# Kernel optimization log

Hardware: AMD Instinct MI355X
Metric: run time of the kernel (lower is better)

## Reference

```python
import jax, jax.numpy as jnp
import numpy as np
from jax import lax

I, H, C = 1086, 16, 15


def _lstm_layer(x, w_ih, w_hh, b):
    # x: [B, T, in], w_ih: [4H, in], w_hh: [4H, H], b: [4H]  (b = b_ih + b_hh)
    B = x.shape[0]
    Hd = w_hh.shape[1]
    # precompute the big input projection outside the scan
    pre = jnp.einsum('bti,gi->btg', x, w_ih) + b  # [B, T, 4H]

    def step(carry, pt):
        h, c = carry
        gates = pt + h @ w_hh.T  # [B, 4H]
        i, f, g, o = jnp.split(gates, 4, axis=-1)  # torch gate order i,f,g,o
        i = jax.nn.sigmoid(i)
        f = jax.nn.sigmoid(f)
        g = jnp.tanh(g)
        o = jax.nn.sigmoid(o)
        c = f * c + i * g
        h = o * jnp.tanh(c)
        return (h, c), h

    h0 = jnp.zeros((B, Hd), x.dtype)
    c0 = jnp.zeros((B, Hd), x.dtype)
    _, ys = lax.scan(step, (h0, c0), jnp.swapaxes(pre, 0, 1))
    return jnp.swapaxes(ys, 0, 1)  # [B, T, H]


def setup_inputs() -> dict:
    key = jax.random.key(0)
    ks = jax.random.split(key, 20)
    s = 1.0 / np.sqrt(H)  # torch LSTM/Linear default init scale
    x = jax.random.normal(ks[0], (256, 200, I), dtype=jnp.float32)

    def w(k, shape):
        return jax.random.uniform(k, shape, jnp.float32, -s, s)

    inp = {'x': x}
    ins = [I, H, H, H]  # lstm1 layer0/1, lstm2 layer0/1
    names = ['l0a', 'l0b', 'l1a', 'l1b']
    ki = 1
    for n, d_in in zip(names, ins):
        inp['w_ih_' + n] = w(ks[ki], (4 * H, d_in)); ki += 1
        inp['w_hh_' + n] = w(ks[ki], (4 * H, H)); ki += 1
        inp['b_' + n] = w(ks[ki], (4 * H,)); ki += 1
    inp['w_fc1'] = w(ks[ki], (H, H)); ki += 1
    inp['b_fc1'] = w(ks[ki], (H,)); ki += 1
    inp['w_fc2'] = w(ks[ki], (C, H)); ki += 1
    inp['b_fc2'] = w(ks[ki], (C,))
    return inp


def reference(x, w_ih_l0a, w_hh_l0a, b_l0a, w_ih_l0b, w_hh_l0b, b_l0b,
              w_ih_l1a, w_hh_l1a, b_l1a, w_ih_l1b, w_hh_l1b, b_l1b,
              w_fc1, b_fc1, w_fc2, b_fc2):
    # lstm1 (2 layers), dropout between layers is identity in eval mode
    out = _lstm_layer(x, w_ih_l0a, w_hh_l0a, b_l0a)
    out = _lstm_layer(out, w_ih_l0b, w_hh_l0b, b_l0b)
    # lstm2 (2 layers)
    out = _lstm_layer(out, w_ih_l1a, w_hh_l1a, b_l1a)
    out = _lstm_layer(out, w_ih_l1b, w_hh_l1b, b_l1b)
    h_last = out[:, -1, :]  # [B, H]
    h = jax.nn.relu(h_last @ w_fc1.T + b_fc1)
    logits = h @ w_fc2.T + b_fc2  # [B, C]
    return jax.nn.softmax(logits, axis=1)
```

## Files before the change

kernel.cpp:

```cpp
#include <hip/hip_runtime.h>

#define T_STEPS 200
#define IN_DIM 1086
#define KTILES 34
#define M_TOTAL 51200

using f32x4v = __attribute__((ext_vector_type(4))) float;
using bf16x8 = __attribute__((ext_vector_type(8))) short;
using u32x4  = __attribute__((ext_vector_type(4))) unsigned int;
typedef unsigned uv2 __attribute__((ext_vector_type(2)));

#if __has_builtin(__builtin_amdgcn_permlane16_swap) && __has_builtin(__builtin_amdgcn_permlane32_swap)
#define HAVE_PERMLANE_SWAP 1
#else
#define HAVE_PERMLANE_SWAP 0
#endif

#if __has_builtin(__builtin_amdgcn_exp2f)
#define EXP2F(x) __builtin_amdgcn_exp2f(x)
#else
#define EXP2F(x) exp2f(x)
#endif

__device__ __forceinline__ float rl_f(float v, int lane) {
    return __uint_as_float((unsigned)__builtin_amdgcn_readlane((int)__float_as_uint(v), lane));
}

__global__ __launch_bounds__(256) void prepack_w(
    const float* __restrict__ W,
    unsigned short* __restrict__ Wh, unsigned short* __restrict__ Wl)
{
    int idx = blockIdx.x * 256 + threadIdx.x;
    if (idx >= KTILES * 4 * 64 * 8) return;
    int j = idx & 7;
    int n = (idx >> 3) & 63;
    int k = (idx >> 9) * 8 + j;
    float v = (k < IN_DIM) ? W[n * IN_DIM + k] : 0.0f;
    unsigned u = __float_as_uint(v);
    unsigned hi = u & 0xffff0000u;
    float lo = v - __uint_as_float(hi);
    Wh[idx] = (unsigned short)(u >> 16);
    Wl[idx] = (unsigned short)(__float_as_uint(lo) >> 16);
}

__device__ __forceinline__ void cvt_hilo(const float a[8], bf16x8& hv, bf16x8& lv) {
    union { u32x4 u; bf16x8 v; } H, L;
    #pragma unroll
    for (int p = 0; p < 4; ++p) {
        float a0 = a[2 * p], a1 = a[2 * p + 1];
        unsigned u0 = __float_as_uint(a0), u1 = __float_as_uint(a1);
        unsigned h0 = u0 & 0xffff0000u, h1 = u1 & 0xffff0000u;
        H.u[p] = (u0 >> 16) | h1;
        float l0 = a0 - __uint_as_float(h0);
        float l1 = a1 - __uint_as_float(h1);
        L.u[p] = (__float_as_uint(l0) >> 16) | (__float_as_uint(l1) & 0xffff0000u);
    }
    hv = H.v; lv = L.v;
}

__global__ __launch_bounds__(64) void pre0_gemm(
    const float* __restrict__ X,
    const unsigned short* __restrict__ Wh, const unsigned short* __restrict__ Wl,
    const float* __restrict__ bias, float* __restrict__ out)
{
    const int lane = threadIdx.x;
    const int fr = lane & 15;
    const int kg = lane >> 4;
    const long m0 = (long)blockIdx.x * 32;

    const float* xr0 = X + (m0 + fr) * (long)IN_DIM;
    const float* xr1 = X + (m0 + 16 + fr) * (long)IN_DIM;

    f32x4v acc[2][4];
    #pragma unroll
    for (int mf = 0; mf < 2; ++mf)
        #pragma unroll
        for (int nf = 0; nf < 4; ++nf)
            #pragma unroll
            for (int r = 0; r < 4; ++r) acc[mf][nf][r] = 0.0f;

    for (int kt = 0; kt < KTILES; ++kt) {
        const int kb = kt * 32 + kg * 8;

        float a0[8], a1[8];
        if (kt < KTILES - 1) {
            #pragma unroll
            for (int q = 0; q < 4; ++q) {
                float2 t0 = *(const float2*)(xr0 + kb + 2 * q);
                float2 t1 = *(const float2*)(xr1 + kb + 2 * q);
                a0[2 * q] = t0.x; a0[2 * q + 1] = t0.y;
                a1[2 * q] = t1.x; a1[2 * q + 1] = t1.y;
            }
        } else {
            #pragma unroll
            for (int j = 0; j < 8; ++j) {
                int k = kb + j;
                a0[j] = (k < IN_DIM) ? xr0[k] : 0.0f;
                a1[j] = (k < IN_DIM) ? xr1[k] : 0.0f;
            }
        }

        const long bbase = (long)(kt * 4 + kg) * 64 * 8;
        bf16x8 bh[4], bl[4];
        #pragma unroll
        for (int nf = 0; nf < 4; ++nf) {
            bh[nf] = *(const bf16x8*)(Wh + bbase + (nf * 16 + fr) * 8);
            bl[nf] = *(const bf16x8*)(Wl + bbase + (nf * 16 + fr) * 8);
        }

        bf16x8 ah0, al0, ah1, al1;
        cvt_hilo(a0, ah0, al0);
        cvt_hilo(a1, ah1, al1);

        #pragma unroll
        for (int nf = 0; nf < 4; ++nf) {
            acc[0][nf] = __builtin_amdgcn_mfma_f32_16x16x32_bf16(ah0, bh[nf], acc[0][nf], 0, 0, 0);
            acc[0][nf] = __builtin_amdgcn_mfma_f32_16x16x32_bf16(al0, bh[nf], acc[0][nf], 0, 0, 0);
            acc[0][nf] = __builtin_amdgcn_mfma_f32_16x16x32_bf16(ah0, bl[nf], acc[0][nf], 0, 0, 0);
            acc[1][nf] = __builtin_amdgcn_mfma_f32_16x16x32_bf16(ah1, bh[nf], acc[1][nf], 0, 0, 0);
            acc[1][nf] = __builtin_amdgcn_mfma_f32_16x16x32_bf16(al1, bh[nf], acc[1][nf], 0, 0, 0);
            acc[1][nf] = __builtin_amdgcn_mfma_f32_16x16x32_bf16(ah1, bl[nf], acc[1][nf], 0, 0, 0);
        }
    }

    float bvv[4];
    #pragma unroll
    for (int nf = 0; nf < 4; ++nf) bvv[nf] = bias[nf * 16 + fr];
    #pragma unroll
    for (int mf = 0; mf < 2; ++mf)
        #pragma unroll
        for (int nf = 0; nf < 4; ++nf)
            #pragma unroll
            for (int r = 0; r < 4; ++r) {
                long row = m0 + mf * 16 + kg * 4 + r;
                out[row * 64 + nf * 16 + fr] = acc[mf][nf][r] + bvv[nf];
            }
}

__global__ __launch_bounds__(256) void mega_scan(
    const float* __restrict__ pre0, const float* __restrict__ whh0,
    const float* __restrict__ wih1, const float* __restrict__ whh1, const float* __restrict__ b1,
    const float* __restrict__ wih2, const float* __restrict__ whh2, const float* __restrict__ b2,
    const float* __restrict__ wih3, const float* __restrict__ whh3, const float* __restrict__ b3,
    const float* __restrict__ w_fc1, const float* __restrict__ b_fc1,
    const float* __restrict__ w_fc2, const float* __restrict__ b_fc2,
    float* __restrict__ out)
{
    __shared__ float buf[3][T_STEPS][16];

    const int b    = blockIdx.x;
    const int tid  = threadIdx.x;
    const int g    = tid & 63;
    const int wv   = tid >> 6;

    bool sel16 = false, sel32 = false;
#if HAVE_PERMLANE_SWAP
    {
        uv2 q16 = __builtin_amdgcn_permlane16_swap((unsigned)g, (unsigned)g, false, false);
        sel16 = (__builtin_amdgcn_readfirstlane((int)q16[1]) == 16);
        uv2 q32 = __builtin_amdgcn_permlane32_swap((unsigned)g, (unsigned)g, false, false);
        sel32 = (__builtin_amdgcn_readfirstlane((int)q32[1]) == 32);
    }
#endif

    const float* wih = nullptr; const float* whh; const float* bias = nullptr;
    if      (wv == 0) { whh = whh0; }
    else if (wv == 1) { wih = wih1; whh = whh1; bias = b1; }
    else if (wv == 2) { wih = wih2; whh = whh2; bias = b2; }
    else              { wih = wih3; whh = whh3; bias = b3; }

    float whh_r[16];
    #pragma unroll
    for (int q = 0; q < 4; ++q)
        *(float4*)&whh_r[q * 4] = *(const float4*)&whh[g * 16 + q * 4];
    float wih_r[16]; float bg = 0.0f;
    if (wv) {
        #pragma unroll
        for (int q = 0; q < 4; ++q)
            *(float4*)&wih_r[q * 4] = *(const float4*)&wih[g * 16 + q * 4];
        bg = bias[g];
    }

    const float* pb = pre0 + (long)b * T_STEPS * 64 + g;
    float pc = 0.0f, p1 = 0.0f, p2 = 0.0f;
    if (wv == 0) { pc = pb[0]; p1 = pb[64]; p2 = pb[128]; }

    float hs[16];
    #pragma unroll
    for (int k = 0; k < 16; ++k) hs[k] = 0.0f;
    float c = 0.0f;

    const int q4 = g >> 4;
    const float escale = (q4 == 2) ? -2.8853900817779268f : -1.4426950408889634f;
    const float am = (q4 == 2) ? 2.0f : 1.0f;
    const float aa = (q4 == 2) ? -1.0f : 0.0f;

    for (int tau = 0; tau < T_STEPS + 3; ++tau) {
        __syncthreads();
        const int t = tau - wv;
        if (t >= 0 && t < T_STEPS) {
            float xr[16];
            if (wv) {
                #pragma unroll
                for (int q = 0; q < 4; ++q)
                    *(float4*)&xr[q * 4] = *(const float4*)&buf[wv - 1][t][q * 4];
            }
            float r0 = fmaf(whh_r[0], hs[0], wv ? bg : pc);
            float r1 = whh_r[1] * hs[1];
            float r2 = whh_r[2] * hs[2];
            float r3 = whh_r[3] * hs[3];
            #pragma unroll
            for (int k = 4; k < 16; k += 4) {
                r0 = fmaf(whh_r[k + 0], hs[k + 0], r0);
                r1 = fmaf(whh_r[k + 1], hs[k + 1], r1);
                r2 = fmaf(whh_r[k + 2], hs[k + 2], r2);
                r3 = fmaf(whh_r[k + 3], hs[k + 3], r3);
            }
            float acc = (r0 + r1) + (r2 + r3);
            if (wv) {
                float p0 = wih_r[0] * xr[0];
                float q1 = wih_r[1] * xr[1];
                float q2 = wih_r[2] * xr[2];
                float q3 = wih_r[3] * xr[3];
                #pragma unroll
                for (int k = 4; k < 16; k += 4) {
                    p0 = fmaf(wih_r[k + 0], xr[k + 0], p0);
                    q1 = fmaf(wih_r[k + 1], xr[k + 1], q1);
                    q2 = fmaf(wih_r[k + 2], xr[k + 2], q2);
                    q3 = fmaf(wih_r[k + 3], xr[k + 3], q3);
                }
                acc += (p0 + q1) + (q2 + q3);
            }
            float e = EXP2F(escale * acc);
            float s = __builtin_amdgcn_rcpf(1.0f + e);
            float a = fmaf(am, s, aa);
#if HAVE_PERMLANE_SWAP
            unsigned au = __float_as_uint(a);
            uv2 r16 = __builtin_amdgcn_permlane16_swap(au, au, false, false);
            uv2 r32 = __builtin_amdgcn_permlane32_swap(au, au, false, false);
            unsigned fvu = sel16 ? r16[1] : r16[0];
            unsigned gvu = sel32 ? r32[1] : r32[0];
            uv2 r48 = __builtin_amdgcn_permlane16_swap(gvu, gvu, false, false);
            unsigned ovu = sel16 ? r48[1] : r48[0];
            float fv = __uint_as_float(fvu);
            float gv = __uint_as_float(gvu);
            float ov = __uint_as_float(ovu);
#else
            float fv = __shfl_xor(a, 16, 64);
            float gv = __shfl_xor(a, 32, 64);
            float ov = __shfl_xor(a, 48, 64);
#endif
            c = fmaf(fv, c, a * gv);
            float e2 = EXP2F(-2.8853900817779268f * c);
            float s2 = __builtin_amdgcn_rcpf(1.0f + e2);
            float hn = fmaf(ov + ov, s2, -ov);
            if (wv < 3 && g < 16) buf[wv][t][g] = hn;
            #pragma unroll
            for (int k = 0; k < 16; ++k) hs[k] = rl_f(hn, k);
            if (wv == 0) {
                pc = p1; p1 = p2;
                int tn = t + 3; tn = tn < T_STEPS ? tn : T_STEPS - 1;
                p2 = pb[(long)tn * 64];
            }
        }
    }

    if (wv == 3 && g < 16) {
        float a1 = b_fc1[g];
        #pragma unroll
        for (int k = 0; k < 16; ++k) a1 = fmaf(w_fc1[g * 16 + k], hs[k], a1);
        a1 = fmaxf(a1, 0.0f);
        float h1[16];
        #pragma unroll
        for (int k = 0; k < 16; ++k) h1[k] = rl_f(a1, k);
        float lg = -3.0e38f;
        if (g < 15) {
            lg = b_fc2[g];
            #pragma unroll
            for (int k = 0; k < 16; ++k) lg = fmaf(w_fc2[g * 16 + k], h1[k], lg);
        }
        float mx = lg;
        #pragma unroll
        for (int d = 8; d >= 1; d >>= 1) mx = fmaxf(mx, __shfl_xor(mx, d, 16));
        float ev = (g < 15) ? EXP2F(1.4426950408889634f * (lg - mx)) : 0.0f;
        float sm = ev;
        #pragma unroll
        for (int d = 8; d >= 1; d >>= 1) sm += __shfl_xor(sm, d, 16);
        if (g < 15) out[b * 15 + g] = ev * __builtin_amdgcn_rcpf(sm);
    }
}

extern "C" void kernel_launch(void* const* d_in, const int* in_sizes, int n_in,
                              void* d_out, int out_size, void* d_ws, size_t ws_size,
                              hipStream_t stream) {
    const float* x    = (const float*)d_in[0];
    const float* wih0 = (const float*)d_in[1];
    const float* whh0 = (const float*)d_in[2];
    const float* b0   = (const float*)d_in[3];
    const float* wih1 = (const float*)d_in[4];
    const float* whh1 = (const float*)d_in[5];
    const float* b1   = (const float*)d_in[6];
    const float* wih2 = (const float*)d_in[7];
    const float* whh2 = (const float*)d_in[8];
    const float* b2   = (const float*)d_in[9];
    const float* wih3 = (const float*)d_in[10];
    const float* whh3 = (const float*)d_in[11];
    const float* b3   = (const float*)d_in[12];
    const float* wfc1 = (const float*)d_in[13];
    const float* bfc1 = (const float*)d_in[14];
    const float* wfc2 = (const float*)d_in[15];
    const float* bfc2 = (const float*)d_in[16];

    float* pre0 = (float*)d_ws;
    unsigned short* Wh = (unsigned short*)((char*)d_ws + 13107200);
    unsigned short* Wl = (unsigned short*)((char*)d_ws + 13107200 + 139264);

    prepack_w<<<dim3((KTILES * 4 * 64 * 8 + 255) / 256), dim3(256), 0, stream>>>(wih0, Wh, Wl);
    pre0_gemm<<<dim3(M_TOTAL / 32), dim3(64), 0, stream>>>(x, Wh, Wl, b0, pre0);
    mega_scan<<<dim3(256), dim3(256), 0, stream>>>(pre0, whh0,
        wih1, whh1, b1, wih2, whh2, b2, wih3, whh3, b3,
        wfc1, bfc1, wfc2, bfc2, (float*)d_out);
}
```

Measured before the change: 166.6 us.

## Stage X and weight tiles through swizzled LDS in the input-projection GEMM

The input-projection GEMM goes from one-wave blocks of 32 rows to 256-thread blocks of 64 rows. Each k-tile of X and of the packed bf16 hi/lo weights is loaded cooperatively into shared memory, with an XOR swizzle on the A tile to avoid bank conflicts. Each wave then reads its 16-row slice and the shared weights from LDS. This is meant to coalesce the strided global reads of X and to share the weight fetch across four waves, at the cost of two barriers per k-tile and no double buffering.

```diff
diff --git a/kernel.cpp b/kernel.cpp
--- a/kernel.cpp
+++ b/kernel.cpp
@@ -5,9 +5,10 @@
 #define KTILES 34
 #define M_TOTAL 51200
 
-using f32x4v = __attribute__((ext_vector_type(4))) float;
-using bf16x8 = __attribute__((ext_vector_type(8))) short;
-using u32x4  = __attribute__((ext_vector_type(4))) unsigned int;
+using f32x4v  = __attribute__((ext_vector_type(4))) float;
+using bf16x8  = __attribute__((ext_vector_type(8))) short;
+using u32x4   = __attribute__((ext_vector_type(4))) unsigned int;
+using ushort8 = __attribute__((ext_vector_type(8))) unsigned short;
 typedef unsigned uv2 __attribute__((ext_vector_type(2)));
 
 #if __has_builtin(__builtin_amdgcn_permlane16_swap) && __has_builtin(__builtin_amdgcn_permlane32_swap)
@@ -43,7 +44,7 @@
     Wl[idx] = (unsigned short)(__float_as_uint(lo) >> 16);
 }
 
-__device__ __forceinline__ void cvt_hilo(const float a[8], bf16x8& hv, bf16x8& lv) {
+__device__ __forceinline__ void cvt_hilo(const float (&a)[8], bf16x8& hv, bf16x8& lv) {
     union { u32x4 u; bf16x8 v; } H, L;
     #pragma unroll
     for (int p = 0; p < 4; ++p) {
@@ -58,68 +59,77 @@
     hv = H.v; lv = L.v;
 }
 
-__global__ __launch_bounds__(64) void pre0_gemm(
+__global__ __launch_bounds__(256) void pre0_gemm_v3(
     const float* __restrict__ X,
     const unsigned short* __restrict__ Wh, const unsigned short* __restrict__ Wl,
     const float* __restrict__ bias, float* __restrict__ out)
 {
-    const int lane = threadIdx.x;
-    const int fr = lane & 15;
-    const int kg = lane >> 4;
-    const long m0 = (long)blockIdx.x * 32;
-
-    const float* xr0 = X + (m0 + fr) * (long)IN_DIM;
-    const float* xr1 = X + (m0 + 16 + fr) * (long)IN_DIM;
-
-    f32x4v acc[2][4];
-    #pragma unroll
-    for (int mf = 0; mf < 2; ++mf)
-        #pragma unroll
-        for (int nf = 0; nf < 4; ++nf)
-            #pragma unroll
-            for (int r = 0; r < 4; ++r) acc[mf][nf][r] = 0.0f;
+    __shared__ float As[64 * 32];
+    __shared__ unsigned short BsH[2048];
+    __shared__ unsigned short BsL[2048];
+
+    const int tid  = threadIdx.x;
+    const int lane = tid & 63;
+    const int wv   = tid >> 6;
+    const int fr   = lane & 15;
+    const int kg   = lane >> 4;
+    const long m0  = (long)blockIdx.x * 64;
+
+    const int row0 = tid >> 4;
+    const int cch  = (tid >> 1) & 7;
+    const int half = tid & 1;
+    const int ldsA0 = row0 * 128 + ((cch ^ (row0 & 7)) << 4) + half * 8;
+    const bool tailskip = (tid & 15) == 15;
+    const float* xsrc = X + (m0 + row0) * (long)IN_DIM + (tid & 15) * 2;
+    char* aB = (char*)As;
+
+    f32x4v acc[4];
+    #pragma unroll
+    for (int nf = 0; nf < 4; ++nf)
+        #pragma unroll
+        for (int r = 0; r < 4; ++r) acc[nf][r] = 0.0f;
 
     for (int kt = 0; kt < KTILES; ++kt) {
-        const int kb = kt * 32 + kg * 8;
-
-        float a0[8], a1[8];
-        if (kt < KTILES - 1) {
-            #pragma unroll
-            for (int q = 0; q < 4; ++q) {
-                float2 t0 = *(const float2*)(xr0 + kb + 2 * q);
-                float2 t1 = *(const float2*)(xr1 + kb + 2 * q);
-                a0[2 * q] = t0.x; a0[2 * q + 1] = t0.y;
-                a1[2 * q] = t1.x; a1[2 * q + 1] = t1.y;
-            }
-        } else {
-            #pragma unroll
-            for (int j = 0; j < 8; ++j) {
-                int k = kb + j;
-                a0[j] = (k < IN_DIM) ? xr0[k] : 0.0f;
-                a1[j] = (k < IN_DIM) ? xr1[k] : 0.0f;
-            }
-        }
-
-        const long bbase = (long)(kt * 4 + kg) * 64 * 8;
+        const bool tail = (kt == KTILES - 1);
+        __syncthreads();
+
+        float2 av[4];
+        #pragma unroll
+        for (int i = 0; i < 4; ++i) {
+            float2 v;
+            if (tail && tailskip) { v.x = 0.0f; v.y = 0.0f; }
+            else v = *(const float2*)(xsrc + (long)i * 16 * IN_DIM + kt * 32);
+            av[i] = v;
+        }
+        ushort8 bhv = *(const ushort8*)(Wh + kt * 2048 + tid * 8);
+        ushort8 blv = *(const ushort8*)(Wl + kt * 2048 + tid * 8);
+        #pragma unroll
+        for (int i = 0; i < 4; ++i)
+            *(float2*)(aB + ldsA0 + i * 2048) = av[i];
+        *(ushort8*)(BsH + tid * 8) = bhv;
+        *(ushort8*)(BsL + tid * 8) = blv;
+        __syncthreads();
+
+        const int r = wv * 16 + fr;
+        const int s = fr & 7;
+        const float* pa1 = As + r * 32 + ((((2 * kg)    ) ^ s) << 2);
+        const float* pa2 = As + r * 32 + ((((2 * kg) | 1) ^ s) << 2);
+        float a[8];
+        *(f32x4v*)&a[0] = *(const f32x4v*)pa1;
+        *(f32x4v*)&a[4] = *(const f32x4v*)pa2;
+        bf16x8 ah, al;
+        cvt_hilo(a, ah, al);
         bf16x8 bh[4], bl[4];
         #pragma unroll
         for (int nf = 0; nf < 4; ++nf) {
-            bh[nf] = *(const bf16x8*)(Wh + bbase + (nf * 16 + fr) * 8);
-            bl[nf] = *(const bf16x8*)(Wl + bbase + (nf * 16 + fr) * 8);
-        }
-
-        bf16x8 ah0, al0, ah1, al1;
-        cvt_hilo(a0, ah0, al0);
-        cvt_hilo(a1, ah1, al1);
-
+            bh[nf] = *(const bf16x8*)(BsH + (kg * 64 + nf * 16 + fr) * 8);
+            bl[nf] = *(const bf16x8*)(BsL + (kg * 64 + nf * 16 + fr) * 8);
+        }
         #pragma unroll
         for (int nf = 0; nf < 4; ++nf) {
-            acc[0][nf] = __builtin_amdgcn_mfma_f32_16x16x32_bf16(ah0, bh[nf], acc[0][nf], 0, 0, 0);
-            acc[0][nf] = __builtin_amdgcn_mfma_f32_16x16x32_bf16(al0, bh[nf], acc[0][nf], 0, 0, 0);
-            acc[0][nf] = __builtin_amdgcn_mfma_f32_16x16x32_bf16(ah0, bl[nf], acc[0][nf], 0, 0, 0);
-            acc[1][nf] = __builtin_amdgcn_mfma_f32_16x16x32_bf16(ah1, bh[nf], acc[1][nf], 0, 0, 0);
-            acc[1][nf] = __builtin_amdgcn_mfma_f32_16x16x32_bf16(al1, bh[nf], acc[1][nf], 0, 0, 0);
-            acc[1][nf] = __builtin_amdgcn_mfma_f32_16x16x32_bf16(ah1, bl[nf], acc[1][nf], 0, 0, 0);
+            acc[nf] = __builtin_amdgcn_mfma_f32_16x16x32_bf16(ah, bh[nf], acc[nf], 0, 0, 0);
+            acc[nf] = __builtin_amdgcn_mfma_f32_16x16x32_bf16(al, bh[nf], acc[nf], 0, 0, 0);
+            acc[nf] = __builtin_amdgcn_mfma_f32_16x16x32_bf16(ah, bl[nf], acc[nf], 0, 0, 0);
         }
     }
 
@@ -127,14 +137,12 @@
     #pragma unroll
     for (int nf = 0; nf < 4; ++nf) bvv[nf] = bias[nf * 16 + fr];
     #pragma unroll
-    for (int mf = 0; mf < 2; ++mf)
-        #pragma unroll
-        for (int nf = 0; nf < 4; ++nf)
-            #pragma unroll
-            for (int r = 0; r < 4; ++r) {
-                long row = m0 + mf * 16 + kg * 4 + r;
-                out[row * 64 + nf * 16 + fr] = acc[mf][nf][r] + bvv[nf];
-            }
+    for (int nf = 0; nf < 4; ++nf)
+        #pragma unroll
+        for (int rr = 0; rr < 4; ++rr) {
+            long row = m0 + wv * 16 + kg * 4 + rr;
+            out[row * 64 + nf * 16 + fr] = acc[nf][rr] + bvv[nf];
+        }
 }
 
 __global__ __launch_bounds__(256) void mega_scan(
@@ -316,7 +324,7 @@
     unsigned short* Wl = (unsigned short*)((char*)d_ws + 13107200 + 139264);
 
     prepack_w<<<dim3((KTILES * 4 * 64 * 8 + 255) / 256), dim3(256), 0, stream>>>(wih0, Wh, Wl);
-    pre0_gemm<<<dim3(M_TOTAL / 32), dim3(64), 0, stream>>>(x, Wh, Wl, b0, pre0);
+    pre0_gemm_v3<<<dim3(M_TOTAL / 64), dim3(256), 0, stream>>>(x, Wh, Wl, b0, pre0);
     mega_scan<<<dim3(256), dim3(256), 0, stream>>>(pre0, whh0,
         wih1, whh1, b1, wih2, whh2, b2, wih3, whh3, b3,
         wfc1, bfc1, wfc2, bfc2, (float*)d_out);
```

Result: faster. 162.5 us (-2.4%).
